# Kernel optimization log

Measured on AMD Instinct MI355X. Metric: run time of the kernel, lower is better.

The kernel has to match this reference:

```python
import jax, jax.numpy as jnp
import numpy as np

HEADS = 24
HEAD_DIM = 128
HIDDEN = HEADS * HEAD_DIM          # 3072
MLP_DIM = int(HIDDEN * 4.0)        # 12288
EPS = 1e-6


def _layernorm(x, eps=EPS):
    mu = jnp.mean(x, axis=-1, keepdims=True)
    var = jnp.mean(jnp.square(x - mu), axis=-1, keepdims=True)
    return (x - mu) * jax.lax.rsqrt(var + eps)


def _rmsnorm(x, w, eps=EPS):
    var = jnp.mean(jnp.square(x), axis=-1, keepdims=True)
    return x * jax.lax.rsqrt(var + eps) * w


def _apply_rope_transposed(x, freqs_cis):
    # x: [B, S_img, H, Dh]; freqs_cis: [S_img, 2*Dh]
    cos, sin = jnp.split(freqs_cis[:, None, :], 2, axis=-1)  # each [S_img, 1, Dh]
    xr = x.reshape(*x.shape[:-1], -1, 2)                      # interleaved pairs
    x_real, x_imag = xr[..., 0], xr[..., 1]
    x_rot = jnp.stack([-x_imag, x_real], axis=-1).reshape(x.shape)
    return x * cos + x_rot * sin


def setup_inputs() -> dict:
    key = jax.random.key(0)
    ks = jax.random.split(key, 20)
    B, S_IMG, S_TXT = 1, 2048, 256
    s = 0.02
    inp = {
        "hidden_states": jax.random.normal(ks[0], (B, S_IMG, HIDDEN), jnp.float32),
        "encoder_hidden_states": jax.random.normal(ks[1], (B, S_TXT, HIDDEN), jnp.float32),
        "temb": jax.random.normal(ks[2], (B, HIDDEN), jnp.float32),
        "freqs_cis": jax.random.uniform(ks[3], (S_IMG, 2 * HEAD_DIM), jnp.float32),
        # AdaLN: Linear(hidden, 3*hidden)
        "w_norm": jax.random.normal(ks[4], (HIDDEN, 3 * HIDDEN), jnp.float32) * s,
        "b_norm": jnp.zeros((3 * HIDDEN,), jnp.float32),
        # attention projections (bias=True)
        "wq": jax.random.normal(ks[5], (HIDDEN, HIDDEN), jnp.float32) * s,
        "bq": jnp.zeros((HIDDEN,), jnp.float32),
        "wk": jax.random.normal(ks[6], (HIDDEN, HIDDEN), jnp.float32) * s,
        "bk": jnp.zeros((HIDDEN,), jnp.float32),
        "wv": jax.random.normal(ks[7], (HIDDEN, HIDDEN), jnp.float32) * s,
        "bv": jnp.zeros((HIDDEN,), jnp.float32),
        # QK RMSNorm weights over head_dim
        "nq_w": jnp.ones((HEAD_DIM,), jnp.float32),
        "nk_w": jnp.ones((HEAD_DIM,), jnp.float32),
        # parallel MLP branch
        "w_mlp": jax.random.normal(ks[8], (HIDDEN, MLP_DIM), jnp.float32) * s,
        "b_mlp": jnp.zeros((MLP_DIM,), jnp.float32),
        # proj_out: Linear(hidden + mlp_dim, hidden)
        "w_out": jax.random.normal(ks[9], (HIDDEN + MLP_DIM, HIDDEN), jnp.float32) * s,
        "b_out": jnp.zeros((HIDDEN,), jnp.float32),
    }
    return inp


def reference(hidden_states, encoder_hidden_states, temb, freqs_cis,
              w_norm, b_norm, wq, bq, wk, bk, wv, bv, nq_w, nk_w,
              w_mlp, b_mlp, w_out, b_out):
    B = hidden_states.shape[0]
    T = encoder_hidden_states.shape[1]  # text_seq_length

    x = jnp.concatenate([hidden_states, encoder_hidden_states], axis=1)  # [B,S,D]
    residual = x

    # AdaLayerNormZeroSingle
    emb = jax.nn.silu(temb) @ w_norm + b_norm          # [B, 3D]
    emb = emb[:, None, :]                              # [B, 1, 3D]
    shift, scale, gate = jnp.split(emb, 3, axis=-1)    # each [B,1,D]
    nx = _layernorm(x) * (1.0 + scale) + shift         # [B,S,D]

    # parallel MLP branch
    mlp = jax.nn.gelu(nx @ w_mlp + b_mlp, approximate=True)  # [B,S,MLP]

    # attention: q/k/v over full (img+txt) normed sequence
    q = (nx @ wq + bq).reshape(B, -1, HEADS, HEAD_DIM)
    k = (nx @ wk + bk).reshape(B, -1, HEADS, HEAD_DIM)
    v = (nx @ wv + bv).reshape(B, -1, HEADS, HEAD_DIM)
    q = _rmsnorm(q, nq_w)
    k = _rmsnorm(k, nk_w)

    # transposed RoPE on image tokens only
    q = jnp.concatenate([_apply_rope_transposed(q[:, :-T], freqs_cis), q[:, -T:]], axis=1)
    k = jnp.concatenate([_apply_rope_transposed(k[:, :-T], freqs_cis), k[:, -T:]], axis=1)

    # full (non-varlen) scaled dot-product attention
    scores = jnp.einsum("bqhd,bkhd->bhqk", q, k) / np.sqrt(HEAD_DIM).astype(np.float32)
    probs = jax.nn.softmax(scores, axis=-1)
    attn = jnp.einsum("bhqk,bkhd->bqhd", probs, v).reshape(B, -1, HIDDEN)

    # concat attention + mlp, project, gated residual
    h = jnp.concatenate([attn, mlp], axis=2)           # [B,S,D+MLP]
    h = gate * (h @ w_out + b_out) + residual          # [B,S,D]

    return h[:, :-T, :], h[:, -T:, :]
```

## Files before the change

### kernel.cpp

```cpp
#include <hip/hip_runtime.h>
#include <hip/hip_bf16.h>

typedef unsigned short u16;
typedef short s16x8 __attribute__((ext_vector_type(8)));
typedef float f32x4 __attribute__((ext_vector_type(4)));
typedef int   i32x4 __attribute__((ext_vector_type(4)));
typedef u16   u16x4 __attribute__((ext_vector_type(4)));

#define HEADS  24
#define HD     128
#define HIDDEN 3072
#define MLPD   12288
#define NTOK   2304
#define SIMG   2048
#define NEMB   9216
#define CATD   15360
#define QKVD   9216
#define FUSEN  21504
#define LN_EPS 1e-6f
#define MB     9

__device__ __forceinline__ u16 f2us(float f){
  __hip_bfloat16 h = __float2bfloat16(f);
  return *reinterpret_cast<u16*>(&h);
}
__device__ __forceinline__ float us2f(u16 u){
  __hip_bfloat16 h;
  *reinterpret_cast<u16*>(&h) = u;
  return __bfloat162float(h);
}
__device__ __forceinline__ float gelu_tanh(float x){
  float y = 0.7978845608028654f*(x + 0.044715f*x*x*x);
  y = fminf(fmaxf(y, -12.f), 12.f);
  float e = __expf(-2.f*y);
  float t = (1.f - e) / (1.f + e);
  return 0.5f*x*(1.0f + t);
}
__device__ __forceinline__ void gload16(const u16* g, u16* l){
  __builtin_amdgcn_global_load_lds(
      (const __attribute__((address_space(1))) void*)g,
      (__attribute__((address_space(3))) void*)l, 16, 0, 0);
}
#define BAR() do{ asm volatile("":::"memory"); __builtin_amdgcn_s_barrier(); asm volatile("":::"memory"); }while(0)
#define VMW_(n) asm volatile("s_waitcnt vmcnt(" #n ")":::"memory")
#define VMW(n) VMW_(n)
#define VMC0() asm volatile("s_waitcnt vmcnt(0)":::"memory")

__global__ __launch_bounds__(256)
void emb_partial(const float* __restrict__ temb, const float* __restrict__ wn,
                 float* __restrict__ partial)
{
  __shared__ float ls[384];
  int tid = threadIdx.x;
  int kb = blockIdx.y * 384;
  for (int i = tid; i < 384; i += 256){
    float t = temb[kb + i];
    ls[i] = t / (1.0f + __expf(-t));
  }
  __syncthreads();
  int j = blockIdx.x*256 + tid;
  const float* wp = wn + (size_t)kb*NEMB + j;
  float acc = 0.f;
  #pragma unroll 8
  for (int i = 0; i < 384; i++){ acc = fmaf(ls[i], wp[0], acc); wp += NEMB; }
  partial[blockIdx.y*NEMB + j] = acc;
}

__global__ __launch_bounds__(256)
void emb_reduce(const float* __restrict__ partial, const float* __restrict__ bn,
                float* __restrict__ emb)
{
  int j = blockIdx.x*256 + threadIdx.x;
  float s = bn[j];
  #pragma unroll
  for (int r = 0; r < 8; r++) s += partial[r*NEMB + j];
  emb[j] = s;
}

__global__ __launch_bounds__(256)
void ln_mod(const float* __restrict__ hs, const float* __restrict__ ehs,
            const float* __restrict__ emb, u16* __restrict__ nx)
{
  int row = blockIdx.x;
  const float* x = (row < SIMG) ? hs + (size_t)row*HIDDEN
                                : ehs + (size_t)(row - SIMG)*HIDDEN;
  int tid = threadIdx.x;
  float vals[12];
  float s = 0.f, ss = 0.f;
  #pragma unroll
  for (int i = 0; i < 3; i++){
    float4 v = *reinterpret_cast<const float4*>(x + i*1024 + tid*4);
    vals[i*4+0]=v.x; vals[i*4+1]=v.y; vals[i*4+2]=v.z; vals[i*4+3]=v.w;
    s += v.x+v.y+v.z+v.w;
    ss += v.x*v.x + v.y*v.y + v.z*v.z + v.w*v.w;
  }
  #pragma unroll
  for (int d = 1; d < 64; d <<= 1){ s += __shfl_xor(s, d); ss += __shfl_xor(ss, d); }
  __shared__ float red[8];
  if ((tid & 63) == 0){ red[tid>>6] = s; red[4 + (tid>>6)] = ss; }
  __syncthreads();
  s  = red[0]+red[1]+red[2]+red[3];
  ss = red[4]+red[5]+red[6]+red[7];
  float mu = s * (1.0f/HIDDEN);
  float var = ss * (1.0f/HIDDEN) - mu*mu;
  float rs = rsqrtf(var + LN_EPS);
  #pragma unroll
  for (int i = 0; i < 3; i++){
    int col = i*1024 + tid*4;
    u16x4 o;
    #pragma unroll
    for (int j = 0; j < 4; j++){
      float nv = (vals[i*4+j] - mu) * rs;
      float outv = nv * (1.0f + emb[HIDDEN + col + j]) + emb[col + j];
      o[j] = f2us(outv);
    }
    *reinterpret_cast<u16x4*>(nx + (size_t)row*HIDDEN + col) = o;
  }
}

__global__ __launch_bounds__(256)
void transpose_w(const float* __restrict__ W, u16* __restrict__ Wt,
                 int K, int N, int ldt, int noff)
{
  __shared__ float t[64][65];
  const int tid = threadIdx.x;
  const int kb = blockIdx.y * 64, nb = blockIdx.x * 64;
  #pragma unroll
  for (int i = 0; i < 4; i++){
    int row = (tid >> 4) + i*16;
    int c4  = (tid & 15) * 4;
    float4 v = *reinterpret_cast<const float4*>(W + (size_t)(kb+row)*N + nb + c4);
    t[row][c4] = v.x; t[row][c4+1] = v.y; t[row][c4+2] = v.z; t[row][c4+3] = v.w;
  }
  __syncthreads();
  int n  = tid >> 2;
  int kc = (tid & 3) * 16;
  u16 tmp[16];
  #pragma unroll
  for (int j = 0; j < 16; j++) tmp[j] = f2us(t[kc+j][n]);
  u16* dst = Wt + (size_t)(noff + nb + n)*ldt + kb + kc;
  *reinterpret_cast<i32x4*>(dst)     = *reinterpret_cast<const i32x4*>(tmp);
  *reinterpret_cast<i32x4*>(dst + 8) = *reinterpret_cast<const i32x4*>(tmp + 8);
}

template<int EPI>
__global__ __launch_bounds__(512, 2)
void gemm8(const u16* __restrict__ A_, int lda,
           const u16* __restrict__ Bt_, int ldb,
           int K, int N, int kspl,
           const float* __restrict__ b0, const float* __restrict__ b1,
           const float* __restrict__ b2, const float* __restrict__ b3,
           u16* __restrict__ qkvo, u16* __restrict__ hcat,
           float* __restrict__ outf)
{
  extern __shared__ __align__(16) u16 lds[];
  const int tid = threadIdx.x, lane = tid & 63, wid = tid >> 6;
  const int l15 = lane & 15, lhi = lane >> 4;
  const int wm = wid >> 2, wn = wid & 3;
  const int NK = K / 64;

  const u16* Ag = A_  + (size_t)blockIdx.z * kspl;
  const u16* Bg = Bt_ + (size_t)blockIdx.z * kspl;

  const int nwg = gridDim.x;
  int orig = blockIdx.x;
  int qq = nwg >> 3, rr = nwg & 7;
  int xcd = orig & 7, loc = orig >> 3;
  int wg = (xcd < rr ? xcd*(qq+1) : rr*(qq+1) + (xcd-rr)*qq) + loc;
  const int m0 = (wg % MB) * 256;
  const int n0 = (wg / MB) * 256;

  const u16 *gA0, *gA1, *gB0, *gB1;
  {
    size_t offA[2], offB[2];
    #pragma unroll
    for (int q = 0; q < 2; q++){
      int Lb = q*8192 + tid*16;
      int r  = Lb >> 7;
      int gp = (Lb >> 4) & 7;
      int g  = gp ^ (r & 7);
      int row = 2*r + (g >> 2);
      int ke  = (g & 3) * 8;
      offA[q] = (size_t)(m0 + row)*lda + ke;
      offB[q] = (size_t)(n0 + row)*ldb + ke;
    }
    gA0 = Ag + offA[0]; gA1 = Ag + offA[1];
    gB0 = Bg + offB[0]; gB1 = Bg + offB[1];
  }
  u16* dA0 = lds + tid*8;
  u16* dA1 = lds + 4096 + tid*8;
  u16* dB0 = lds + 32768 + tid*8;
  u16* dB1 = lds + 36864 + tid*8;

  const char* pa[8];
  const char* pb[4];
  {
    const char* LB = (const char*)lds;
    #pragma unroll
    for (int c = 0; c < 2; c++)
      #pragma unroll
      for (int mf = 0; mf < 4; mf++){
        int R = wm*128 + c*64 + mf*16 + l15;
        int off = (R>>1)*128 + (((((R&1)<<2)|lhi) ^ ((R>>1)&7))*16);
        pa[c*4+mf] = LB + off;
      }
    #pragma unroll
    for (int nf = 0; nf < 4; nf++){
      int R = wn*64 + nf*16 + l15;
      int off = (R>>1)*128 + (((((R&1)<<2)|lhi) ^ ((R>>1)&7))*16);
      pb[nf] = LB + 65536 + off;
    }
  }

  f32x4 acc[8][4];
  #pragma unroll
  for (int i = 0; i < 8; i++)
    #pragma unroll
    for (int j = 0; j < 4; j++){ f32x4 z = {0.f,0.f,0.f,0.f}; acc[i][j] = z; }

  #define LD8(P_) (*reinterpret_cast<const s16x8*>(P_))
  #define MFMA_BLK(A0_) do{                                                    \
    _Pragma("unroll") for (int mf_=0; mf_<4; mf_++)                            \
      _Pragma("unroll") for (int nf_=0; nf_<4; nf_++)                          \
        acc[(A0_)+mf_][nf_] = __builtin_amdgcn_mfma_f32_16x16x32_bf16(         \
            af[(A0_)+mf_], bf[nf_], acc[(A0_)+mf_][nf_], 0, 0, 0); }while(0)

  #define KBODY(P_,DOE_,DOL_,EOFF_,LOFF_,V2_,V4_) do{                          \
    constexpr int CA0 = (P_)?32768:0, CA1 = (P_)?49152:16384;                  \
    constexpr int ERE = (P_)?8192:24576, LRE = (P_)?16384:0;                   \
    s16x8 af[8], bf[4];                                                        \
                         \
    _Pragma("unroll") for (int i_=0;i_<8;i_++) af[i_] = LD8(pa[i_]+CA0);       \
    _Pragma("unroll") for (int i_=0;i_<4;i_++) bf[i_] = LD8(pb[i_]+CA0);       \
    if (DOE_){ gload16(gA0+(EOFF_), dA0+ERE); gload16(gA1+(EOFF_), dA1+ERE); } \
    __builtin_amdgcn_s_setprio(1); MFMA_BLK(0); __builtin_amdgcn_s_setprio(0); \
    BAR();                                                                     \
                               \
    if (DOE_){ gload16(gB0+(EOFF_), dB0+ERE); gload16(gB1+(EOFF_), dB1+ERE); } \
    __builtin_amdgcn_s_setprio(1); MFMA_BLK(4); __builtin_amdgcn_s_setprio(0); \
    VMW(V2_); BAR();                                                           \
                                                         \
    _Pragma("unroll") for (int i_=0;i_<8;i_++) af[i_] = LD8(pa[i_]+CA1);       \
    _Pragma("unroll") for (int i_=0;i_<4;i_++) bf[i_] = LD8(pb[i_]+CA1);       \
    if (DOL_){ gload16(gA0+(LOFF_), dA0+LRE); gload16(gA1+(LOFF_), dA1+LRE); } \
    __builtin_amdgcn_s_setprio(1); MFMA_BLK(0); __builtin_amdgcn_s_setprio(0); \
    BAR();                                                                     \
                                                         \
    if (DOL_){ gload16(gB0+(LOFF_), dB0+LRE); gload16(gB1+(LOFF_), dB1+LRE); } \
    __builtin_amdgcn_s_setprio(1); MFMA_BLK(4); __builtin_amdgcn_s_setprio(0); \
    VMW(V4_); BAR();                                                           \
  }while(0)

  gload16(gA0,    dA0);         gload16(gA1,    dA1);
  gload16(gB0,    dB0);         gload16(gB1,    dB1);
  gload16(gA0+32, dA0+8192);    gload16(gA1+32, dA1+8192);
  gload16(gB0+32, dB0+8192);    gload16(gB1+32, dB1+8192);
  gload16(gA0+64, dA0+16384);   gload16(gA1+64, dA1+16384);
  gload16(gB0+64, dB0+16384);   gload16(gB1+64, dB1+16384);
  VMW(8);
  BAR();

  for (int jj = 0; jj + 3 < NK; jj += 2){
    KBODY(0, 1, 1,  96, 128, 8, 8);
    KBODY(1, 1, 1, 160, 192, 8, 8);
    gA0 += 128; gA1 += 128; gB0 += 128; gB1 += 128;
  }
  KBODY(0, 1, 0, 96, 0, 8, 4);
  KBODY(1, 0, 0, 0, 0, 0, 0);
  VMC0();

  #undef KBODY
  #undef MFMA_BLK
  #undef LD8

  #pragma unroll
  for (int a = 0; a < 8; a++){
    #pragma unroll
    for (int nf = 0; nf < 4; nf++){
      int col = n0 + wn*64 + nf*16 + l15;
      #pragma unroll
      for (int r = 0; r < 4; r++){
        int row = m0 + wm*128 + a*16 + lhi*4 + r;
        float v = acc[a][nf][r];
        if constexpr (EPI == 0){
          if (col < QKVD){
            const float* bp = b0; int c = col;
            if (c >= 6144){ bp = b2; c -= 6144; }
            else if (c >= 3072){ bp = b1; c -= 3072; }
            qkvo[(size_t)row*QKVD + col] = f2us(v + bp[c]);
          } else {
            int c2 = col - QKVD;
            hcat[(size_t)row*CATD + HIDDEN + c2] = f2us(gelu_tanh(v + b3[c2]));
          }
        } else {
          outf[(size_t)blockIdx.z*NTOK*HIDDEN + (size_t)row*HIDDEN + col] = v;
        }
      }
    }
  }
}

__global__ __launch_bounds__(256)
void reduce_out(const float* __restrict__ part, const float* __restrict__ bout,
                const float* __restrict__ emb,
                const float* __restrict__ hs, const float* __restrict__ ehs,
                float* __restrict__ outp)
{
  int row = blockIdx.x;
  const float* res = (row < SIMG) ? hs + (size_t)row*HIDDEN
                                  : ehs + (size_t)(row - SIMG)*HIDDEN;
  #pragma unroll
  for (int i = 0; i < 3; i++){
    int col = i*1024 + threadIdx.x*4;
    float4 a = *reinterpret_cast<const float4*>(part + (size_t)row*HIDDEN + col);
    float4 b = *reinterpret_cast<const float4*>(part + (size_t)NTOK*HIDDEN + (size_t)row*HIDDEN + col);
    float4 rr = *reinterpret_cast<const float4*>(res + col);
    float4 bb = *reinterpret_cast<const float4*>(bout + col);
    float4 gg = *reinterpret_cast<const float4*>(emb + 2*HIDDEN + col);
    float4 o;
    o.x = gg.x*(a.x+b.x+bb.x) + rr.x;
    o.y = gg.y*(a.y+b.y+bb.y) + rr.y;
    o.z = gg.z*(a.z+b.z+bb.z) + rr.z;
    o.w = gg.w*(a.w+b.w+bb.w) + rr.w;
    *reinterpret_cast<float4*>(outp + (size_t)row*HIDDEN + col) = o;
  }
}

__global__ __launch_bounds__(256)
void qk_post(u16* __restrict__ qkv,
             const float* __restrict__ nqw, const float* __restrict__ nkw,
             const float* __restrict__ fc)
{
  int rid = blockIdx.x*4 + (threadIdx.x >> 6);
  int lane = threadIdx.x & 63;
  int isK = rid >= NTOK*HEADS;
  int r = isK ? rid - NTOK*HEADS : rid;
  int token = r / HEADS, head = r % HEADS;
  u16* p = qkv + (size_t)token*QKVD + (isK ? HIDDEN : 0) + head*HD + lane*2;
  unsigned int u = *reinterpret_cast<unsigned int*>(p);
  float v0 = us2f((u16)(u & 0xffff));
  float v1 = us2f((u16)(u >> 16));
  float ss = v0*v0 + v1*v1;
  #pragma unroll
  for (int d = 1; d < 64; d <<= 1) ss += __shfl_xor(ss, d);
  float rs = rsqrtf(ss * (1.0f/HD) + LN_EPS);
  const float* wv = isK ? nkw : nqw;
  v0 *= rs * wv[lane*2];
  v1 *= rs * wv[lane*2+1];
  if (token < SIMG){
    const float* f = fc + (size_t)token*(2*HD);
    float c0 = f[lane*2],      c1 = f[lane*2+1];
    float s0 = f[HD + lane*2], s1 = f[HD + lane*2+1];
    float o0 = v0*c0 - v1*s0;
    float o1 = v1*c1 + v0*s1;
    v0 = o0; v1 = o1;
  }
  unsigned int uo = (unsigned int)f2us(v0) | ((unsigned int)f2us(v1) << 16);
  *reinterpret_cast<unsigned int*>(p) = uo;
}

__global__ __launch_bounds__(256)
void attn_kernel(const u16* __restrict__ qkv, u16* __restrict__ hcat)
{
  __shared__ __align__(16) u16 Qs[64][136];
  __shared__ __align__(16) u16 Ks[64][136];
  __shared__ __align__(16) u16 Vt[128][72];
  __shared__ __align__(16) u16 Ps[64][72];

  const int tid = threadIdx.x, lane = tid & 63, w = tid >> 6;
  const int head = blockIdx.y, qb = blockIdx.x;
  const int l15 = lane & 15, lhi = lane >> 4;
  const int q0 = qb * 64;
  const float scale = 0.08838834764831845f;

  #pragma unroll
  for (int i = 0; i < 4; i++){
    int c = tid + 256*i;
    int row = c >> 4, d0 = (c & 15) * 8;
    i32x4 vv = *reinterpret_cast<const i32x4*>(qkv + (size_t)(q0+row)*QKVD + head*HD + d0);
    *reinterpret_cast<i32x4*>(&Qs[row][d0]) = vv;
  }

  f32x4 O[8];
  #pragma unroll
  for (int i = 0; i < 8; i++){ f32x4 z = {0.f,0.f,0.f,0.f}; O[i] = z; }
  float mrow[4], lrow[4];
  #pragma unroll
  for (int r = 0; r < 4; r++){ mrow[r] = -1e30f; lrow[r] = 0.f; }

  for (int kv0 = 0; kv0 < NTOK; kv0 += 64){
    #pragma unroll
    for (int i = 0; i < 4; i++){
      int c = tid + 256*i;
      int row = c >> 4, d0 = (c & 15) * 8;
      i32x4 vv = *reinterpret_cast<const i32x4*>(qkv + (size_t)(kv0+row)*QKVD + HIDDEN + head*HD + d0);
      *reinterpret_cast<i32x4*>(&Ks[row][d0]) = vv;
    }
    #pragma unroll
    for (int i = 0; i < 4; i++){
      int c = tid + 256*i;
      int kvr = c >> 4, d0 = (c & 15) * 8;
      i32x4 vv = *reinterpret_cast<const i32x4*>(qkv + (size_t)(kv0+kvr)*QKVD + 2*HIDDEN + head*HD + d0);
      const u16* pv = reinterpret_cast<const u16*>(&vv);
      #pragma unroll
      for (int j = 0; j < 8; j++){
        int d = d0 + j;
        int col = (((kvr>>3) ^ ((d>>3)&7)) << 3) | (kvr & 7);
        Vt[d][col] = pv[j];
      }
    }
    __syncthreads();

    f32x4 S[4];
    #pragma unroll
    for (int nf = 0; nf < 4; nf++){ f32x4 z = {0.f,0.f,0.f,0.f}; S[nf] = z; }
    #pragma unroll
    for (int ks = 0; ks < 4; ks++){
      s16x8 a = *reinterpret_cast<const s16x8*>(&Qs[w*16 + l15][ks*32 + lhi*8]);
      #pragma unroll
      for (int nf = 0; nf < 4; nf++){
        s16x8 b = *reinterpret_cast<const s16x8*>(&Ks[nf*16 + l15][ks*32 + lhi*8]);
        S[nf] = __builtin_amdgcn_mfma_f32_16x16x32_bf16(a, b, S[nf], 0, 0, 0);
      }
    }
    #pragma unroll
    for (int nf = 0; nf < 4; nf++)
      #pragma unroll
      for (int r = 0; r < 4; r++) S[nf][r] *= scale;

    float fsc[4];
    #pragma unroll
    for (int r = 0; r < 4; r++){
      float mx = -1e30f;
      #pragma unroll
      for (int nf = 0; nf < 4; nf++) mx = fmaxf(mx, S[nf][r]);
      #pragma unroll
      for (int d = 1; d < 16; d <<= 1) mx = fmaxf(mx, __shfl_xor(mx, d));
      float mn = fmaxf(mrow[r], mx);
      float f = __expf(mrow[r] - mn);
      mrow[r] = mn; fsc[r] = f;
      float lsum = 0.f;
      int prow = w*16 + lhi*4 + r;
      #pragma unroll
      for (int nf = 0; nf < 4; nf++){
        float pvl = __expf(S[nf][r] - mn);
        lsum += pvl;
        int pcol = nf*16 + l15;
        int col = (((pcol>>3) ^ (prow&7)) << 3) | (pcol & 7);
        Ps[prow][col] = f2us(pvl);
      }
      #pragma unroll
      for (int d = 1; d < 16; d <<= 1) lsum += __shfl_xor(lsum, d);
      lrow[r] = lrow[r]*f + lsum;
    }
    #pragma unroll
    for (int nf = 0; nf < 8; nf++)
      #pragma unroll
      for (int r = 0; r < 4; r++) O[nf][r] *= fsc[r];
    __syncthreads();

    #pragma unroll
    for (int ks = 0; ks < 2; ks++){
      int prow = w*16 + l15;
      int cb = ((ks*4 + lhi) ^ (prow & 7)) << 3;
      s16x8 a = *reinterpret_cast<const s16x8*>(&Ps[prow][cb]);
      #pragma unroll
      for (int nf = 0; nf < 8; nf++){
        int d = nf*16 + l15;
        int vb = ((ks*4 + lhi) ^ ((d>>3)&7)) << 3;
        s16x8 b = *reinterpret_cast<const s16x8*>(&Vt[d][vb]);
        O[nf] = __builtin_amdgcn_mfma_f32_16x16x32_bf16(a, b, O[nf], 0, 0, 0);
      }
    }
    __syncthreads();
  }

  #pragma unroll
  for (int nf = 0; nf < 8; nf++){
    #pragma unroll
    for (int r = 0; r < 4; r++){
      int row = q0 + w*16 + lhi*4 + r;
      int col = head*HD + nf*16 + l15;
      hcat[(size_t)row*CATD + col] = f2us(O[nf][r] / lrow[r]);
    }
  }
}

extern "C" void kernel_launch(void* const* d_in, const int* in_sizes, int n_in,
                              void* d_out, int out_size, void* d_ws, size_t ws_size,
                              hipStream_t stream)
{
  const float* hs    = (const float*)d_in[0];
  const float* ehs   = (const float*)d_in[1];
  const float* temb  = (const float*)d_in[2];
  const float* fc    = (const float*)d_in[3];
  const float* wnorm = (const float*)d_in[4];
  const float* bnorm = (const float*)d_in[5];
  const float* wq    = (const float*)d_in[6];
  const float* bq    = (const float*)d_in[7];
  const float* wk    = (const float*)d_in[8];
  const float* bk    = (const float*)d_in[9];
  const float* wv    = (const float*)d_in[10];
  const float* bv    = (const float*)d_in[11];
  const float* nqw   = (const float*)d_in[12];
  const float* nkw   = (const float*)d_in[13];
  const float* wmlp  = (const float*)d_in[14];
  const float* bmlp  = (const float*)d_in[15];
  const float* wout  = (const float*)d_in[16];
  const float* bout  = (const float*)d_in[17];
  float* outp = (float*)d_out;

  char* ws = (char*)d_ws;
  float* emb  = (float*)ws;
  float* part = (float*)(ws + 36864);
  u16* nx     = (u16*)(ws + 36864 + 294912);
  u16* qkv    = nx  + (size_t)NTOK*HIDDEN;
  u16* hcat   = qkv + (size_t)NTOK*QKVD;
  u16* Wt     = hcat + (size_t)NTOK*CATD;
  float* partial = (float*)nx;

  hipFuncSetAttribute((const void*)gemm8<0>, hipFuncAttributeMaxDynamicSharedMemorySize, 131072);
  hipFuncSetAttribute((const void*)gemm8<1>, hipFuncAttributeMaxDynamicSharedMemorySize, 131072);

  emb_partial<<<dim3(36,8), 256, 0, stream>>>(temb, wnorm, part);
  emb_reduce<<<36, 256, 0, stream>>>(part, bnorm, emb);
  ln_mod<<<NTOK, 256, 0, stream>>>(hs, ehs, emb, nx);

  transpose_w<<<dim3(48,48), 256, 0, stream>>>(wq,   Wt, HIDDEN, HIDDEN, HIDDEN, 0);
  transpose_w<<<dim3(48,48), 256, 0, stream>>>(wk,   Wt, HIDDEN, HIDDEN, HIDDEN, HIDDEN);
  transpose_w<<<dim3(48,48), 256, 0, stream>>>(wv,   Wt, HIDDEN, HIDDEN, HIDDEN, 2*HIDDEN);
  transpose_w<<<dim3(192,48), 256, 0, stream>>>(wmlp, Wt, HIDDEN, MLPD, HIDDEN, QKVD);

  gemm8<0><<<dim3((FUSEN/256)*MB, 1, 1), 512, 131072, stream>>>(
      nx, HIDDEN, Wt, HIDDEN, HIDDEN, FUSEN, 0,
      bq, bk, bv, bmlp, qkv, hcat, nullptr);

  transpose_w<<<dim3(48,240), 256, 0, stream>>>(wout, Wt, CATD, HIDDEN, CATD, 0);

  qk_post<<<(2*NTOK*HEADS)/4, 256, 0, stream>>>(qkv, nqw, nkw, fc);
  attn_kernel<<<dim3(NTOK/64, HEADS), 256, 0, stream>>>(qkv, hcat);

  gemm8<1><<<dim3((HIDDEN/256)*MB, 1, 2), 512, 131072, stream>>>(
      hcat, CATD, Wt, CATD, CATD/2, HIDDEN, CATD/2,
      nullptr, nullptr, nullptr, nullptr, nullptr, nullptr, partial);

  reduce_out<<<NTOK, 256, 0, stream>>>(partial, bout, emb, hs, ehs, outp);
}
```

Measured before the change: 979.7 us.

## Double-buffer GEMM fragments in registers and prefetch attention K/V tiles

After: 1.033 ms. 5.4% more time.

```diff
diff --git a/kernel.cpp b/kernel.cpp
--- a/kernel.cpp
+++ b/kernel.cpp
@@ -6,6 +6,8 @@
 typedef float f32x4 __attribute__((ext_vector_type(4)));
 typedef int   i32x4 __attribute__((ext_vector_type(4)));
 typedef u16   u16x4 __attribute__((ext_vector_type(4)));
+typedef unsigned int u32;
+typedef u32   u32x2 __attribute__((ext_vector_type(2)));
 
 #define HEADS  24
 #define HD     128
@@ -192,24 +194,13 @@
   u16* dB0 = lds + 32768 + tid*8;
   u16* dB1 = lds + 36864 + tid*8;
 
-  const char* pa[8];
-  const char* pb[4];
+  const char *pa0, *pb0;
   {
     const char* LB = (const char*)lds;
-    #pragma unroll
-    for (int c = 0; c < 2; c++)
-      #pragma unroll
-      for (int mf = 0; mf < 4; mf++){
-        int R = wm*128 + c*64 + mf*16 + l15;
-        int off = (R>>1)*128 + (((((R&1)<<2)|lhi) ^ ((R>>1)&7))*16);
-        pa[c*4+mf] = LB + off;
-      }
-    #pragma unroll
-    for (int nf = 0; nf < 4; nf++){
-      int R = wn*64 + nf*16 + l15;
-      int off = (R>>1)*128 + (((((R&1)<<2)|lhi) ^ ((R>>1)&7))*16);
-      pb[nf] = LB + 65536 + off;
-    }
+    int Ra = wm*128 + l15;
+    pa0 = LB + (Ra>>1)*128 + (((((Ra&1)<<2)|lhi) ^ ((Ra>>1)&7))*16);
+    int Rb = wn*64 + l15;
+    pb0 = LB + 65536 + (Rb>>1)*128 + (((((Rb&1)<<2)|lhi) ^ ((Rb>>1)&7))*16);
   }
 
   f32x4 acc[8][4];
@@ -218,37 +209,33 @@
     #pragma unroll
     for (int j = 0; j < 4; j++){ f32x4 z = {0.f,0.f,0.f,0.f}; acc[i][j] = z; }
 
+  s16x8 afX[8], afY[8], bfX[4], bfY[4];
+
   #define LD8(P_) (*reinterpret_cast<const s16x8*>(P_))
-  #define MFMA_BLK(A0_) do{                                                    \
-    _Pragma("unroll") for (int mf_=0; mf_<4; mf_++)                            \
-      _Pragma("unroll") for (int nf_=0; nf_<4; nf_++)                          \
-        acc[(A0_)+mf_][nf_] = __builtin_amdgcn_mfma_f32_16x16x32_bf16(         \
-            af[(A0_)+mf_], bf[nf_], acc[(A0_)+mf_][nf_], 0, 0, 0); }while(0)
-
-  #define KBODY(P_,DOE_,DOL_,EOFF_,LOFF_,V2_,V4_) do{                          \
-    constexpr int CA0 = (P_)?32768:0, CA1 = (P_)?49152:16384;                  \
-    constexpr int ERE = (P_)?8192:24576, LRE = (P_)?16384:0;                   \
-    s16x8 af[8], bf[4];                                                        \
-                         \
-    _Pragma("unroll") for (int i_=0;i_<8;i_++) af[i_] = LD8(pa[i_]+CA0);       \
-    _Pragma("unroll") for (int i_=0;i_<4;i_++) bf[i_] = LD8(pb[i_]+CA0);       \
-    if (DOE_){ gload16(gA0+(EOFF_), dA0+ERE); gload16(gA1+(EOFF_), dA1+ERE); } \
-    __builtin_amdgcn_s_setprio(1); MFMA_BLK(0); __builtin_amdgcn_s_setprio(0); \
-    BAR();                                                                     \
-                               \
-    if (DOE_){ gload16(gB0+(EOFF_), dB0+ERE); gload16(gB1+(EOFF_), dB1+ERE); } \
-    __builtin_amdgcn_s_setprio(1); MFMA_BLK(4); __builtin_amdgcn_s_setprio(0); \
-    VMW(V2_); BAR();                                                           \
-                                                         \
-    _Pragma("unroll") for (int i_=0;i_<8;i_++) af[i_] = LD8(pa[i_]+CA1);       \
-    _Pragma("unroll") for (int i_=0;i_<4;i_++) bf[i_] = LD8(pb[i_]+CA1);       \
-    if (DOL_){ gload16(gA0+(LOFF_), dA0+LRE); gload16(gA1+(LOFF_), dA1+LRE); } \
-    __builtin_amdgcn_s_setprio(1); MFMA_BLK(0); __builtin_amdgcn_s_setprio(0); \
-    BAR();                                                                     \
-                                                         \
-    if (DOL_){ gload16(gB0+(LOFF_), dB0+LRE); gload16(gB1+(LOFF_), dB1+LRE); } \
-    __builtin_amdgcn_s_setprio(1); MFMA_BLK(4); __builtin_amdgcn_s_setprio(0); \
-    VMW(V4_); BAR();                                                           \
+  #define MFMA_ALL(AF_, BF_) do{                                               \
+    _Pragma("unroll") for (int a_=0;a_<8;a_++)                                 \
+      _Pragma("unroll") for (int nf_=0;nf_<4;nf_++)                            \
+        acc[a_][nf_] = __builtin_amdgcn_mfma_f32_16x16x32_bf16(                \
+            (AF_)[a_], (BF_)[nf_], acc[a_][nf_], 0, 0, 0); }while(0)
+
+  #define PHASE(AFU_,BFU_,AFR_,BFR_,CN_,DORD_,DOI_,RT_,GOFF_,VN_) do{          \
+    if (DORD_){                                                                \
+      _Pragma("unroll") for (int i_=0;i_<4;i_++)                               \
+        BFR_[i_] = LD8(pb0 + (CN_) + i_*1024);                                 \
+      _Pragma("unroll") for (int i_=0;i_<8;i_++)                               \
+        AFR_[i_] = LD8(pa0 + (CN_) + (i_>>2)*4096 + (i_&3)*1024);              \
+    }                                                                          \
+    if (DOI_){                                                                 \
+      gload16(gA0+(GOFF_), dA0+(RT_)*8192); gload16(gA1+(GOFF_), dA1+(RT_)*8192);\
+      gload16(gB0+(GOFF_), dB0+(RT_)*8192); gload16(gB1+(GOFF_), dB1+(RT_)*8192);\
+    }                                                                          \
+    __builtin_amdgcn_s_setprio(1);                                             \
+    MFMA_ALL(AFU_, BFU_);                                                      \
+    __builtin_amdgcn_s_setprio(0);                                             \
+    if (DORD_) __builtin_amdgcn_sched_group_barrier(0x100, 12, 0);             \
+    if (DOI_)  __builtin_amdgcn_sched_group_barrier(0x10, 4, 0);               \
+    __builtin_amdgcn_sched_group_barrier(0x8, 32, 0);                          \
+    VMW(VN_); BAR();                                                           \
   }while(0)
 
   gload16(gA0,    dA0);         gload16(gA1,    dA1);
@@ -257,20 +244,27 @@
   gload16(gB0+32, dB0+8192);    gload16(gB1+32, dB1+8192);
   gload16(gA0+64, dA0+16384);   gload16(gA1+64, dA1+16384);
   gload16(gB0+64, dB0+16384);   gload16(gB1+64, dB1+16384);
-  VMW(8);
+  VMW(4);
   BAR();
+  #pragma unroll
+  for (int i_ = 0; i_ < 4; i_++) bfX[i_] = LD8(pb0 + i_*1024);
+  #pragma unroll
+  for (int i_ = 0; i_ < 8; i_++) afX[i_] = LD8(pa0 + (i_>>2)*4096 + (i_&3)*1024);
 
   for (int jj = 0; jj + 3 < NK; jj += 2){
-    KBODY(0, 1, 1,  96, 128, 8, 8);
-    KBODY(1, 1, 1, 160, 192, 8, 8);
+    PHASE(afX,bfX, afY,bfY, 16384, 1, 1, 3,  96, 4);
+    PHASE(afY,bfY, afX,bfX, 32768, 1, 1, 0, 128, 4);
+    PHASE(afX,bfX, afY,bfY, 49152, 1, 1, 1, 160, 4);
+    PHASE(afY,bfY, afX,bfX,     0, 1, 1, 2, 192, 4);
     gA0 += 128; gA1 += 128; gB0 += 128; gB1 += 128;
   }
-  KBODY(0, 1, 0, 96, 0, 8, 4);
-  KBODY(1, 0, 0, 0, 0, 0, 0);
-  VMC0();
-
-  #undef KBODY
-  #undef MFMA_BLK
+  PHASE(afX,bfX, afY,bfY, 16384, 1, 1, 3, 96, 4);
+  PHASE(afY,bfY, afX,bfX, 32768, 1, 0, 0,  0, 0);
+  PHASE(afX,bfX, afY,bfY, 49152, 1, 0, 0,  0, 0);
+  PHASE(afY,bfY, afX,bfX,     0, 0, 0, 0,  0, 0);
+
+  #undef PHASE
+  #undef MFMA_ALL
   #undef LD8
 
   #pragma unroll
@@ -381,6 +375,33 @@
     *reinterpret_cast<i32x4*>(&Qs[row][d0]) = vv;
   }
 
+  int krow[4], kd0[4];
+  #pragma unroll
+  for (int i = 0; i < 4; i++){ int c = tid + 256*i; krow[i] = c >> 4; kd0[i] = (c & 15)*8; }
+  const int vbase = w*16 + lhi*4;
+  const int vd0   = l15*8;
+  char* vwp = (char*)(&Vt[0][0]) + vd0*144 + (((vbase>>3) ^ ((vd0>>3)&7))*16) + (vbase&7)*2;
+
+  i32x4 kr0, kr1, kr2, kr3, vr0, vr1, vr2, vr3;
+  {
+    const u16* kbp = qkv + HIDDEN + (size_t)head*HD;
+    const u16* vbp = qkv + 2*HIDDEN + (size_t)head*HD;
+    kr0 = *reinterpret_cast<const i32x4*>(kbp + (size_t)(krow[0])*QKVD + kd0[0]);
+    kr1 = *reinterpret_cast<const i32x4*>(kbp + (size_t)(krow[1])*QKVD + kd0[1]);
+    kr2 = *reinterpret_cast<const i32x4*>(kbp + (size_t)(krow[2])*QKVD + kd0[2]);
+    kr3 = *reinterpret_cast<const i32x4*>(kbp + (size_t)(krow[3])*QKVD + kd0[3]);
+    vr0 = *reinterpret_cast<const i32x4*>(vbp + (size_t)(vbase+0)*QKVD + vd0);
+    vr1 = *reinterpret_cast<const i32x4*>(vbp + (size_t)(vbase+1)*QKVD + vd0);
+    vr2 = *reinterpret_cast<const i32x4*>(vbp + (size_t)(vbase+2)*QKVD + vd0);
+    vr3 = *reinterpret_cast<const i32x4*>(vbp + (size_t)(vbase+3)*QKVD + vd0);
+  }
+  __syncthreads();
+
+  s16x8 qf[4];
+  #pragma unroll
+  for (int ks = 0; ks < 4; ks++)
+    qf[ks] = *reinterpret_cast<const s16x8*>(&Qs[w*16 + l15][ks*32 + lhi*8]);
+
   f32x4 O[8];
   #pragma unroll
   for (int i = 0; i < 8; i++){ f32x4 z = {0.f,0.f,0.f,0.f}; O[i] = z; }
@@ -389,38 +410,43 @@
   for (int r = 0; r < 4; r++){ mrow[r] = -1e30f; lrow[r] = 0.f; }
 
   for (int kv0 = 0; kv0 < NTOK; kv0 += 64){
-    #pragma unroll
-    for (int i = 0; i < 4; i++){
-      int c = tid + 256*i;
-      int row = c >> 4, d0 = (c & 15) * 8;
-      i32x4 vv = *reinterpret_cast<const i32x4*>(qkv + (size_t)(kv0+row)*QKVD + HIDDEN + head*HD + d0);
-      *reinterpret_cast<i32x4*>(&Ks[row][d0]) = vv;
-    }
-    #pragma unroll
-    for (int i = 0; i < 4; i++){
-      int c = tid + 256*i;
-      int kvr = c >> 4, d0 = (c & 15) * 8;
-      i32x4 vv = *reinterpret_cast<const i32x4*>(qkv + (size_t)(kv0+kvr)*QKVD + 2*HIDDEN + head*HD + d0);
-      const u16* pv = reinterpret_cast<const u16*>(&vv);
-      #pragma unroll
-      for (int j = 0; j < 8; j++){
-        int d = d0 + j;
-        int col = (((kvr>>3) ^ ((d>>3)&7)) << 3) | (kvr & 7);
-        Vt[d][col] = pv[j];
-      }
+    *reinterpret_cast<i32x4*>(&Ks[krow[0]][kd0[0]]) = kr0;
+    *reinterpret_cast<i32x4*>(&Ks[krow[1]][kd0[1]]) = kr1;
+    *reinterpret_cast<i32x4*>(&Ks[krow[2]][kd0[2]]) = kr2;
+    *reinterpret_cast<i32x4*>(&Ks[krow[3]][kd0[3]]) = kr3;
+    #pragma unroll
+    for (int dd = 0; dd < 8; dd++){
+      u32 a0 = (u32)(dd & 1 ? ((u32)vr0[dd>>1]) >> 16 : ((u32)vr0[dd>>1]) & 0xffff);
+      u32 a1 = (u32)(dd & 1 ? ((u32)vr1[dd>>1]) >> 16 : ((u32)vr1[dd>>1]) & 0xffff);
+      u32 a2 = (u32)(dd & 1 ? ((u32)vr2[dd>>1]) >> 16 : ((u32)vr2[dd>>1]) & 0xffff);
+      u32 a3 = (u32)(dd & 1 ? ((u32)vr3[dd>>1]) >> 16 : ((u32)vr3[dd>>1]) & 0xffff);
+      u32x2 pk; pk[0] = a0 | (a1 << 16); pk[1] = a2 | (a3 << 16);
+      *reinterpret_cast<u32x2*>(vwp + dd*144) = pk;
     }
     __syncthreads();
 
+    if (kv0 + 64 < NTOK){
+      const u16* kbp = qkv + (size_t)(kv0+64)*QKVD + HIDDEN + (size_t)head*HD;
+      const u16* vbp = qkv + (size_t)(kv0+64)*QKVD + 2*HIDDEN + (size_t)head*HD;
+      kr0 = *reinterpret_cast<const i32x4*>(kbp + (size_t)(krow[0])*QKVD + kd0[0]);
+      kr1 = *reinterpret_cast<const i32x4*>(kbp + (size_t)(krow[1])*QKVD + kd0[1]);
+      kr2 = *reinterpret_cast<const i32x4*>(kbp + (size_t)(krow[2])*QKVD + kd0[2]);
+      kr3 = *reinterpret_cast<const i32x4*>(kbp + (size_t)(krow[3])*QKVD + kd0[3]);
+      vr0 = *reinterpret_cast<const i32x4*>(vbp + (size_t)(vbase+0)*QKVD + vd0);
+      vr1 = *reinterpret_cast<const i32x4*>(vbp + (size_t)(vbase+1)*QKVD + vd0);
+      vr2 = *reinterpret_cast<const i32x4*>(vbp + (size_t)(vbase+2)*QKVD + vd0);
+      vr3 = *reinterpret_cast<const i32x4*>(vbp + (size_t)(vbase+3)*QKVD + vd0);
+    }
+
     f32x4 S[4];
     #pragma unroll
     for (int nf = 0; nf < 4; nf++){ f32x4 z = {0.f,0.f,0.f,0.f}; S[nf] = z; }
     #pragma unroll
     for (int ks = 0; ks < 4; ks++){
-      s16x8 a = *reinterpret_cast<const s16x8*>(&Qs[w*16 + l15][ks*32 + lhi*8]);
       #pragma unroll
       for (int nf = 0; nf < 4; nf++){
         s16x8 b = *reinterpret_cast<const s16x8*>(&Ks[nf*16 + l15][ks*32 + lhi*8]);
-        S[nf] = __builtin_amdgcn_mfma_f32_16x16x32_bf16(a, b, S[nf], 0, 0, 0);
+        S[nf] = __builtin_amdgcn_mfma_f32_16x16x32_bf16(qf[ks], b, S[nf], 0, 0, 0);
       }
     }
     #pragma unroll
@@ -457,7 +483,6 @@
     for (int nf = 0; nf < 8; nf++)
       #pragma unroll
       for (int r = 0; r < 4; r++) O[nf][r] *= fsc[r];
-    __syncthreads();
 
     #pragma unroll
     for (int ks = 0; ks < 2; ks++){
```
